# Kernel tuning notes

Measured on AMD Instinct MI355X. Metric: run time of the kernel, lower is better.

## Reference

```python
import jax, jax.numpy as jnp
import numpy as np

B, S = 256, 512
NQ = 1000           # n_skills
MEM, DK, DV, FC = 20, 50, 200, 50  # memory_size, key dim, value dim, final fc dim


def _kaiming(key, shape, fan_in):
    return jax.random.normal(key, shape) * np.float32(np.sqrt(2.0 / fan_in))


def setup_inputs() -> dict:
    key = jax.random.key(0)
    ks = jax.random.split(key, 12)
    q_data = jax.random.randint(ks[0], (B, S), 0, NQ + 1)
    qa_data = jax.random.randint(ks[1], (B, S), 0, 2 * NQ + 1)
    u = jax.random.uniform(ks[2], (B * S,))
    # target: -1 = masked/padding, else binary label (matches target.ge(0) masking)
    target = jnp.where(u < 0.1, -1.0, (u > 0.55).astype(jnp.float32))
    q_embed_w = _kaiming(ks[3], (NQ + 1, DK), DK)
    qa_embed_w = _kaiming(ks[4], (2 * NQ + 1, DV), DV)
    memory_key = _kaiming(ks[5], (MEM, DK), DK)
    init_memory_value = _kaiming(ks[6], (MEM, DV), DV)
    erase_w = _kaiming(ks[7], (DV, DV), DV)
    erase_b = jnp.zeros((DV,), jnp.float32)
    add_w = _kaiming(ks[8], (DV, DV), DV)
    add_b = jnp.zeros((DV,), jnp.float32)
    read_w = _kaiming(ks[9], (DV + FC, FC), DV + FC)
    read_b = jnp.zeros((FC,), jnp.float32)
    pred_w = _kaiming(ks[10], (FC, 1), FC)
    pred_b = jnp.zeros((1,), jnp.float32)
    return dict(q_data=q_data, qa_data=qa_data, target=target,
                q_embed_w=q_embed_w, qa_embed_w=qa_embed_w,
                memory_key=memory_key, init_memory_value=init_memory_value,
                erase_w=erase_w, erase_b=erase_b, add_w=add_w, add_b=add_b,
                read_w=read_w, read_b=read_b, pred_w=pred_w, pred_b=pred_b)


def reference(q_data, qa_data, target, q_embed_w, qa_embed_w, memory_key,
              init_memory_value, erase_w, erase_b, add_w, add_b,
              read_w, read_b, pred_w, pred_b):
    b = q_data.shape[0]
    q_e = q_embed_w[q_data]     # [B,S,DK]
    qa_e = qa_embed_w[qa_data]  # [B,S,DV]
    Mv0 = jnp.broadcast_to(init_memory_value, (b, MEM, DV))

    def step(Mv, xs):
        q_t, qa_t = xs                                        # [B,DK], [B,DV]
        corr = jax.nn.softmax(q_t @ memory_key.T, axis=1)     # [B,MEM] addressing
        read = jnp.einsum('bm,bmd->bd', corr, Mv)             # weighted read
        erase = jax.nn.sigmoid(qa_t @ erase_w + erase_b)      # [B,DV]
        add = jnp.tanh(qa_t @ add_w + add_b)                  # [B,DV]
        w = corr[:, :, None]                                  # [B,MEM,1]
        Mv = Mv * (1.0 - w * erase[:, None, :]) + w * add[:, None, :]
        return Mv, read

    _, reads = jax.lax.scan(step, Mv0, (q_e.transpose(1, 0, 2), qa_e.transpose(1, 0, 2)))
    reads = reads.transpose(1, 0, 2)                          # [B,S,DV]
    x = jnp.concatenate([reads, q_e], axis=-1)                # [B,S,DV+FC]
    h = jnp.tanh(x @ read_w + read_b)                         # [B,S,FC]
    logits = (h @ pred_w + pred_b).reshape(-1)                # [B*S]
    mask = target >= 0.0
    t = jnp.where(mask, target, 0.0)
    # numerically-stable BCE-with-logits, masked mean
    bce = jnp.maximum(logits, 0.0) - logits * t + jnp.log1p(jnp.exp(-jnp.abs(logits)))
    loss = jnp.sum(jnp.where(mask, bce, 0.0)) / jnp.maximum(mask.sum(), 1)
    return loss, jax.nn.sigmoid(logits)
```

## Files before the change

### kernel.cpp

```cpp
#include <hip/hip_runtime.h>
#include <math.h>

#define B_   256
#define S_   512
#define NQ_  1000
#define MEM_ 20
#define DK_  50
#define DV_  200
#define FC_  50
#define RPB  4
#define CHK  16
#define CLEN (S_/CHK)
#define NKS  7
#define XS_STRIDE 232
#define CORR_STRIDE 12
#define NB_EA    ((2*NQ_+1+RPB-1)/RPB)
#define NB_CORR  4
#define NB_WPACK 7
#define NB_HQ    251
#define PREP1_BLOCKS (NB_EA+NB_CORR)
#define MM_BLOCKS (B_*CHK)
#define SCANA_BLOCKS (B_*(CHK-1))
#define SCANA_TOTAL (SCANA_BLOCKS+NB_WPACK+NB_HQ)

typedef __attribute__((ext_vector_type(8))) short bf16x8_t;
typedef __attribute__((ext_vector_type(4))) float f32x4_t;
typedef __attribute__((ext_vector_type(2))) _Float16 f16x2_t;

static __device__ __forceinline__ f16x2_t h2(unsigned u){ return __builtin_bit_cast(f16x2_t, u); }
static __device__ __forceinline__ unsigned h2u(f16x2_t v){ return __builtin_bit_cast(unsigned, v); }
static __device__ __forceinline__ unsigned packh2(float x, float y){
  unsigned short bx = __builtin_bit_cast(unsigned short, (_Float16)x);
  unsigned short by = __builtin_bit_cast(unsigned short, (_Float16)y);
  return (unsigned)bx | ((unsigned)by << 16);
}
static __device__ __forceinline__ f16x2_t pkfma16(f16x2_t a, f16x2_t b, f16x2_t c){
  return __builtin_elementwise_fma(a, b, c);
}

static __device__ __forceinline__ unsigned short f2bf(float f){
  unsigned u = __float_as_uint(f);
  unsigned r = u + 0x7fffu + ((u >> 16) & 1u);
  return (unsigned short)(r >> 16);
}
static __device__ __forceinline__ float ftanh(float x){
  float e = __expf(2.f*x);
  return 1.f - 2.f*__builtin_amdgcn_rcpf(e+1.f);
}
static __device__ __forceinline__ float fsigm(float x){
  return __builtin_amdgcn_rcpf(1.f+__expf(-x));
}

__global__ __launch_bounds__(256) void k_prep1(
    const float* __restrict__ qaw,
    const float* __restrict__ ew, const float* __restrict__ eb,
    const float* __restrict__ aw, const float* __restrict__ ab,
    uint2* __restrict__ eaTab,
    const float* __restrict__ qw, const float* __restrict__ mk,
    unsigned* __restrict__ corrH){
  __shared__ float qa[RPB*DV_];
  int blk = blockIdx.x;
  if(blk < NB_EA){
    int row0 = blk*RPB;
    for(int i=threadIdx.x; i<RPB*DV_; i+=256){
      int r = i/DV_, cc = i - r*DV_;
      int row = row0 + r;
      qa[i] = (row <= 2*NQ_) ? qaw[row*DV_+cc] : 0.f;
    }
    __syncthreads();
    int d = threadIdx.x;
    if(d >= DV_) return;
    float accE[RPB], accA[RPB];
    #pragma unroll
    for(int r=0;r<RPB;++r){ accE[r] = eb[d]; accA[r] = ab[d]; }
    float we0 = ew[d], wa0 = aw[d];
    for(int j=0;j<DV_;++j){
      int jn = (j+1 < DV_) ? j+1 : j;
      float we1 = ew[jn*DV_+d];
      float wa1 = aw[jn*DV_+d];
      #pragma unroll
      for(int r=0;r<RPB;++r){
        float x = qa[r*DV_+j];
        accE[r] = fmaf(x, we0, accE[r]);
        accA[r] = fmaf(x, wa0, accA[r]);
      }
      we0 = we1; wa0 = wa1;
    }
    #pragma unroll
    for(int r=0;r<RPB;++r){
      int row = row0 + r;
      if(row <= 2*NQ_){
        unsigned he = (unsigned)__builtin_bit_cast(unsigned short, (_Float16)fsigm(accE[r]));
        unsigned ha = (unsigned)__builtin_bit_cast(unsigned short, (_Float16)ftanh(accA[r]));
        eaTab[(size_t)row*DV_+d] = make_uint2(he*0x10001u, ha*0x10001u);
      }
    }
  } else {
    int q = (blk-NB_EA)*256 + threadIdx.x;
    if(q > NQ_) return;
    float qv[DK_];
    #pragma unroll
    for(int j=0;j<DK_;++j) qv[j] = qw[q*DK_+j];
    float s[MEM_]; float mx = -1e30f;
    #pragma unroll
    for(int m=0;m<MEM_;++m){
      float acc = 0.f;
      #pragma unroll
      for(int j=0;j<DK_;++j) acc = fmaf(qv[j], mk[m*DK_+j], acc);
      s[m] = acc; mx = fmaxf(mx, acc);
    }
    float sum = 0.f;
    #pragma unroll
    for(int m=0;m<MEM_;++m){ s[m] = __expf(s[m]-mx); sum += s[m]; }
    float inv = __builtin_amdgcn_rcpf(sum);
    #pragma unroll
    for(int i=0;i<MEM_/2;++i)
      corrH[q*CORR_STRIDE+i] = packh2(s[2*i]*inv, s[2*i+1]*inv);
  }
}

__global__ __launch_bounds__(256,8) void k_scanA(const int* __restrict__ qd,
    const int* __restrict__ qad,
    const unsigned* __restrict__ corrH,
    const uint2* __restrict__ eaTab,
    unsigned* __restrict__ ABu,
    const float* __restrict__ qw,
    const float* __restrict__ rw, const float* __restrict__ rb,
    const float* __restrict__ pw,
    unsigned short* __restrict__ WpFrag, float* __restrict__ pwPad,
    float* __restrict__ hq){
  const int blk = blockIdx.x;
  if(blk >= SCANA_BLOCKS){
    int xblk = blk - SCANA_BLOCKS;
    if(xblk < NB_WPACK){
      int ks = xblk;
      int nt = threadIdx.x >> 6;
      int lane = threadIdx.x & 63;
      int quad = lane >> 4, col = lane & 15;
      int n = nt*16 + col;
      unsigned short tmp[8];
      #pragma unroll
      for(int j=0;j<8;++j){
        int k = ks*32 + quad*8 + j;
        tmp[j] = (k < DV_ && n < FC_) ? f2bf(rw[k*FC_+n]) : (unsigned short)0;
      }
      uint4* dst = reinterpret_cast<uint4*>(WpFrag + ((size_t)(ks*4+nt)*64 + lane)*8);
      *dst = *reinterpret_cast<const uint4*>(tmp);
      if(ks == 0 && threadIdx.x < 64)
        pwPad[threadIdx.x] = (threadIdx.x < FC_) ? pw[threadIdx.x] : 0.f;
    } else {
      int idx = (xblk-NB_WPACK)*256 + threadIdx.x;
      int q = idx >> 6, n = idx & 63;
      if(q > NQ_) return;
      float v = 0.f;
      if(n < FC_){
        float acc = rb[n];
        #pragma unroll
        for(int j=0;j<DK_;++j)
          acc = fmaf(qw[q*DK_+j], rw[(DV_+j)*FC_+n], acc);
        v = acc;
      }
      hq[q*64+n] = v;
    }
    return;
  }

  const int b = blk / (CHK-1), c = blk % (CHK-1);
  const int d = threadIdx.x;
  const int dc = (d < DV_) ? d : DV_-1;
  const bool act = (d < DV_);
  const int* __restrict__ qp  = qd  + b*S_ + c*CLEN;
  const int* __restrict__ qap = qad + b*S_ + c*CLEN;

  const f16x2_t one2h = {(_Float16)1.f, (_Float16)1.f};
  f16x2_t A2[MEM_/2], B2[MEM_/2];
  #pragma unroll
  for(int i=0;i<MEM_/2;++i){ A2[i] = one2h; B2[i] = (f16x2_t){(_Float16)0.f,(_Float16)0.f}; }

  int q2   = qp[1];
  int qaT2 = qap[2];
  int qaT3 = qap[3];
  int q1s  = __builtin_amdgcn_readfirstlane(qp[0]);
  const unsigned* cp0 = corrH + q1s*CORR_STRIDE;
  uint4 ca = *(const uint4*)(cp0);
  uint4 cb = *(const uint4*)(cp0+4);
  uint2 cc = *(const uint2*)(cp0+8);
  uint2 ea  = eaTab[(size_t)qap[0]*DV_ + dc];
  uint2 ean = eaTab[(size_t)qap[1]*DV_ + dc];

  #pragma unroll 4
  for(int t=0;t<CLEN;++t){
    int t2 = (t+2 < CLEN) ? t+2 : CLEN-1;
    int t4 = (t+4 < CLEN) ? t+4 : CLEN-1;
    int q3 = qp[t2];
    int qaN = qap[t4];
    int qs = __builtin_amdgcn_readfirstlane(q2);
    const unsigned* cpn_ = corrH + qs*CORR_STRIDE;
    uint4 na = *(const uint4*)(cpn_);
    uint4 nb = *(const uint4*)(cpn_+4);
    uint2 nc = *(const uint2*)(cpn_+8);
    uint2 eann = eaTab[(size_t)qaT2*DV_ + dc];

    const f16x2_t ee = h2(ea.x), aa = h2(ea.y);
    #define UPDA(u, i) { \
      f16x2_t cp = h2(u); \
      f16x2_t al = pkfma16(-cp, ee, one2h); \
      f16x2_t be = cp*aa; \
      A2[i] = A2[i]*al; \
      B2[i] = pkfma16(al, B2[i], be); }
    UPDA(ca.x, 0)  UPDA(ca.y, 1)  UPDA(ca.z, 2)  UPDA(ca.w, 3)
    UPDA(cb.x, 4)  UPDA(cb.y, 5)  UPDA(cb.z, 6)  UPDA(cb.w, 7)
    UPDA(cc.x, 8)  UPDA(cc.y, 9)
    #undef UPDA

    ca=na; cb=nb; cc=nc;
    ea=ean; ean=eann;
    q2=q3; qaT2=qaT3; qaT3=qaN;
  }
  if(act){
    unsigned* base = ABu + ((size_t)(b*(CHK-1) + c)*MEM_)*DV_ + d;
    #pragma unroll
    for(int i=0;i<MEM_/2;++i){
      unsigned a01 = h2u(A2[i]);
      unsigned b01 = h2u(B2[i]);
      base[(size_t)(2*i)*DV_]   = (a01 & 0xffffu) | (b01 << 16);
      base[(size_t)(2*i+1)*DV_] = (a01 >> 16)     | (b01 & 0xffff0000u);
    }
  }
}

__global__ __launch_bounds__(256) void k_prefix(const float* __restrict__ mv0,
    const unsigned* __restrict__ ABu, unsigned* __restrict__ Mv0p){
  int i = blockIdx.x*256 + threadIdx.x;
  if(i >= B_*(MEM_/2)*DV_) return;
  int d = i % DV_;
  int p = (i / DV_) % (MEM_/2);
  int b = i / (DV_*(MEM_/2));
  float MvE = mv0[(2*p)*DV_+d];
  float MvO = mv0[(2*p+1)*DV_+d];
  #pragma unroll
  for(int c=1;c<CHK;++c){
    unsigned vE = ABu[((size_t)(b*(CHK-1) + (c-1))*MEM_ + 2*p)*DV_ + d];
    unsigned vO = ABu[((size_t)(b*(CHK-1) + (c-1))*MEM_ + 2*p+1)*DV_ + d];
    MvE = fmaf((float)h2(vE)[0], MvE, (float)h2(vE)[1]);
    MvO = fmaf((float)h2(vO)[0], MvO, (float)h2(vO)[1]);
    Mv0p[((size_t)(b*CHK + c)*(MEM_/2) + p)*DV_ + d] = packh2(MvE, MvO);
  }
}

__global__ __launch_bounds__(256,8) void k_scan_mm(const int* __restrict__ qd,
    const int* __restrict__ qad,
    const unsigned* __restrict__ corrH,
    const uint2* __restrict__ eaTab,
    const float* __restrict__ mv0,
    const unsigned* __restrict__ Mv0p,
    const unsigned short* __restrict__ WpFrag,
    const float* __restrict__ hq,
    const float* __restrict__ pwPad, const float* __restrict__ pb,
    const float* __restrict__ target,
    float* __restrict__ out, float2* __restrict__ partials){
  __shared__ unsigned short Xs[CLEN*XS_STRIDE];
  __shared__ float sred[2][2][16];
  __shared__ float sbce[4];

  const int blk = blockIdx.x;
  const int b = blk >> 4, c = blk & (CHK-1);
  const int d = threadIdx.x;
  const int dc = (d < DV_) ? d : DV_-1;
  const bool act = (d < DV_);
  const bool padw = (d < 224);
  const int* __restrict__ qp  = qd  + b*S_ + c*CLEN;
  const int* __restrict__ qap = qad + b*S_ + c*CLEN;

  const int wave = threadIdx.x >> 6;
  const int lane = threadIdx.x & 63;
  const int col  = lane & 15, quad = lane >> 4;
  const int rt   = wave & 1;
  const int nh   = wave >> 1;
  const int mbase = rt*16;

  int qpre[4];
  #pragma unroll
  for(int reg=0;reg<4;++reg) qpre[reg] = qp[mbase + quad*4 + reg];

  f16x2_t Mv2[MEM_/2];
  if(c == 0){
    #pragma unroll
    for(int i=0;i<MEM_/2;++i)
      Mv2[i] = (f16x2_t){ (_Float16)mv0[(2*i)*DV_+dc], (_Float16)mv0[(2*i+1)*DV_+dc] };
  } else {
    const unsigned* base = Mv0p + ((size_t)(b*CHK + c)*(MEM_/2))*DV_ + dc;
    #pragma unroll
    for(int i=0;i<MEM_/2;++i)
      Mv2[i] = h2(base[(size_t)i*DV_]);
  }

  int q2   = qp[1];
  int qaT2 = qap[2];
  int qaT3 = qap[3];
  int q1s  = __builtin_amdgcn_readfirstlane(qp[0]);
  const unsigned* cp0 = corrH + q1s*CORR_STRIDE;
  uint4 ca = *(const uint4*)(cp0);
  uint4 cb = *(const uint4*)(cp0+4);
  uint2 cc = *(const uint2*)(cp0+8);
  uint2 ea  = eaTab[(size_t)qap[0]*DV_ + dc];
  uint2 ean = eaTab[(size_t)qap[1]*DV_ + dc];

  #pragma unroll 4
  for(int t=0;t<CLEN;++t){
    int t2 = (t+2 < CLEN) ? t+2 : CLEN-1;
    int t4 = (t+4 < CLEN) ? t+4 : CLEN-1;
    int q3 = qp[t2];
    int qaN = qap[t4];
    int qs = __builtin_amdgcn_readfirstlane(q2);
    const unsigned* cpn_ = corrH + qs*CORR_STRIDE;
    uint4 na = *(const uint4*)(cpn_);
    uint4 nb = *(const uint4*)(cpn_+4);
    uint2 nc = *(const uint2*)(cpn_+8);
    uint2 eann = eaTab[(size_t)qaT2*DV_ + dc];

    const f16x2_t ee = h2(ea.x), aa = h2(ea.y);
    float rd0 = 0.f, rd1 = 0.f;
    #define UPD2(u, i, acc) { \
      f16x2_t cp = h2(u); \
      acc = __builtin_amdgcn_fdot2(cp, Mv2[i], acc, false); \
      f16x2_t tt = pkfma16(-Mv2[i], ee, aa); \
      Mv2[i] = pkfma16(cp, tt, Mv2[i]); }
    UPD2(ca.x, 0, rd0)  UPD2(ca.y, 1, rd1)  UPD2(ca.z, 2, rd0)  UPD2(ca.w, 3, rd1)
    UPD2(cb.x, 4, rd0)  UPD2(cb.y, 5, rd1)  UPD2(cb.z, 6, rd0)  UPD2(cb.w, 7, rd1)
    UPD2(cc.x, 8, rd0)  UPD2(cc.y, 9, rd1)
    #undef UPD2

    if(padw) Xs[t*XS_STRIDE + d] = act ? f2bf(rd0+rd1) : (unsigned short)0;

    ca=na; cb=nb; cc=nc;
    ea=ean; ean=eann;
    q2=q3; qaT2=qaT3; qaT3=qaN;
  }
  __syncthreads();

  float hqv[4][2];
  #pragma unroll
  for(int reg=0;reg<4;++reg)
    #pragma unroll
    for(int j=0;j<2;++j)
      hqv[reg][j] = hq[qpre[reg]*64 + (nh*2+j)*16 + col];

  f32x4_t acc[2];
  acc[0] = (f32x4_t){0.f,0.f,0.f,0.f};
  acc[1] = (f32x4_t){0.f,0.f,0.f,0.f};

  #pragma unroll
  for(int ks=0;ks<NKS;++ks){
    bf16x8_t a = *reinterpret_cast<const bf16x8_t*>(Xs + (mbase+col)*XS_STRIDE + quad*8 + ks*32);
    #pragma unroll
    for(int j=0;j<2;++j){
      int nt = nh*2 + j;
      bf16x8_t bfr = *reinterpret_cast<const bf16x8_t*>(WpFrag + ((size_t)(ks*4+nt)*64 + lane)*8);
      acc[j] = __builtin_amdgcn_mfma_f32_16x16x32_bf16(a, bfr, acc[j], 0, 0, 0);
    }
  }

  float part[4];
  #pragma unroll
  for(int reg=0;reg<4;++reg){
    float s = 0.f;
    #pragma unroll
    for(int j=0;j<2;++j){
      int n = (nh*2+j)*16 + col;
      float h = acc[j][reg] + hqv[reg][j];
      s = fmaf(pwPad[n], ftanh(h), s);
    }
    part[reg] = s;
  }
  #pragma unroll
  for(int off=1; off<16; off<<=1){
    #pragma unroll
    for(int reg=0;reg<4;++reg) part[reg] += __shfl_xor(part[reg], off, 64);
  }
  if(col == 0){
    #pragma unroll
    for(int reg=0;reg<4;++reg) sred[rt][nh][quad*4+reg] = part[reg];
  }
  __syncthreads();

  float bce = 0.f, cnt = 0.f;
  if(nh == 0 && col == 0){
    float pbv = pb[0];
    #pragma unroll
    for(int reg=0;reg<4;++reg){
      int idx = quad*4 + reg;
      int mloc = mbase + idx;
      int row = b*S_ + c*CLEN + mloc;
      float logit = sred[rt][0][idx] + sred[rt][1][idx] + pbv;
      out[1+row] = fsigm(logit);
      float t = target[row];
      if(t >= 0.f){
        cnt += 1.f;
        bce += fmaxf(logit,0.f) - logit*t + log1pf(__expf(-fabsf(logit)));
      }
    }
  }
  bce += __shfl_xor(bce, 16, 64); cnt += __shfl_xor(cnt, 16, 64);
  bce += __shfl_xor(bce, 32, 64); cnt += __shfl_xor(cnt, 32, 64);
  if(lane == 0 && nh == 0){ sbce[wave] = bce; sbce[2+wave] = cnt; }
  __syncthreads();
  if(threadIdx.x == 0)
    partials[blk] = make_float2(sbce[0]+sbce[1], sbce[2]+sbce[3]);
}

__global__ __launch_bounds__(256) void k_fin(const float2* __restrict__ partials,
                                             float* __restrict__ out){
  float bce = 0.f, cnt = 0.f;
  for(int i=threadIdx.x; i<MM_BLOCKS; i+=256){
    float2 p = partials[i];
    bce += p.x; cnt += p.y;
  }
  #pragma unroll
  for(int off=32; off>0; off>>=1){
    bce += __shfl_down(bce, off, 64);
    cnt += __shfl_down(cnt, off, 64);
  }
  __shared__ float sb[4], sc[4];
  int w = threadIdx.x >> 6;
  if((threadIdx.x & 63) == 0){ sb[w] = bce; sc[w] = cnt; }
  __syncthreads();
  if(threadIdx.x == 0){
    float Bt = sb[0]+sb[1]+sb[2]+sb[3];
    float Ct = sc[0]+sc[1]+sc[2]+sc[3];
    out[0] = Bt / fmaxf(Ct, 1.f);
  }
}

extern "C" void kernel_launch(void* const* d_in, const int* in_sizes, int n_in,
                              void* d_out, int out_size, void* d_ws, size_t ws_size,
                              hipStream_t stream){
  const int*   qd     = (const int*)d_in[0];
  const int*   qad    = (const int*)d_in[1];
  const float* target = (const float*)d_in[2];
  const float* qw     = (const float*)d_in[3];
  const float* qaw    = (const float*)d_in[4];
  const float* mk     = (const float*)d_in[5];
  const float* mv0    = (const float*)d_in[6];
  const float* ew     = (const float*)d_in[7];
  const float* eb     = (const float*)d_in[8];
  const float* aw     = (const float*)d_in[9];
  const float* ab     = (const float*)d_in[10];
  const float* rw     = (const float*)d_in[11];
  const float* rb     = (const float*)d_in[12];
  const float* pw     = (const float*)d_in[13];
  const float* pb     = (const float*)d_in[14];
  float* out = (float*)d_out;

  char* ws = (char*)d_ws;
  size_t off = 0;
  float2* partials = (float2*)(ws + off);            off += (size_t)MM_BLOCKS*8;
  unsigned* corrH = (unsigned*)(ws + off);           off += (((size_t)(NQ_+1)*CORR_STRIDE*4 + 255)/256)*256;
  uint2* eaTab    = (uint2*)(ws + off);              off += (((size_t)(2*NQ_+1)*DV_*8 + 255)/256)*256;
  unsigned* ABu   = (unsigned*)(ws + off);           off += (size_t)SCANA_BLOCKS*MEM_*DV_*4;
  unsigned* Mv0p  = (unsigned*)(ws + off);           off += (size_t)MM_BLOCKS*(MEM_/2)*DV_*4;
  unsigned short* WpFrag = (unsigned short*)(ws + off); off += ((size_t)NKS*4*64*8*2 + 255)/256*256;
  float* pwPad    = (float*)(ws + off);              off += 256;
  float* hq       = (float*)(ws + off);              off += (size_t)(NQ_+1)*64*4;

  k_prep1<<<dim3(PREP1_BLOCKS), dim3(256), 0, stream>>>(qaw, ew, eb, aw, ab, eaTab,
                                                        qw, mk, corrH);
  k_scanA<<<dim3(SCANA_TOTAL), dim3(256), 0, stream>>>(qd, qad, corrH, eaTab,
                                                       ABu, qw, rw, rb, pw, WpFrag, pwPad, hq);
  k_prefix<<<dim3((B_*(MEM_/2)*DV_+255)/256), dim3(256), 0, stream>>>(mv0, ABu, Mv0p);
  k_scan_mm<<<dim3(MM_BLOCKS), dim3(256), 0, stream>>>(qd, qad, corrH, eaTab,
                                                       mv0, Mv0p, WpFrag, hq, pwPad, pb, target, out, partials);
  k_fin<<<dim3(1), dim3(256), 0, stream>>>(partials, out);
}
```

Before: 224.1 us.

## Compute erase/add table with bf16 MFMA instead of scalar FMA

Replaces the scalar fp32 per-thread matmul that built the erase/add gate table (2001x200 by 200x400) with a bf16 MFMA kernel. Weights are first packed into MFMA B-fragments (erase and add concatenated along N) in the prep kernel, then a new kernel tiles 32 qa rows per block and applies sigmoid/tanh on the accumulators. This cuts the ALU cost of the table precompute but adds an extra kernel launch and lowers the input precision of the gate computation to bf16.

```diff
diff --git a/kernel.cpp b/kernel.cpp
--- a/kernel.cpp
+++ b/kernel.cpp
@@ -8,17 +8,18 @@
 #define DK_  50
 #define DV_  200
 #define FC_  50
-#define RPB  4
 #define CHK  16
 #define CLEN (S_/CHK)
 #define NKS  7
 #define XS_STRIDE 232
 #define CORR_STRIDE 12
-#define NB_EA    ((2*NQ_+1+RPB-1)/RPB)
+#define EA_NT 28
 #define NB_CORR  4
+#define NB_WPK2  ((NKS*EA_NT+3)/4)
+#define PREP1_BLOCKS (NB_CORR+NB_WPK2)
+#define EA_BLOCKS ((2*NQ_+1+31)/32)
 #define NB_WPACK 7
 #define NB_HQ    251
-#define PREP1_BLOCKS (NB_EA+NB_CORR)
 #define MM_BLOCKS (B_*CHK)
 #define SCANA_BLOCKS (B_*(CHK-1))
 #define SCANA_TOTAL (SCANA_BLOCKS+NB_WPACK+NB_HQ)
@@ -52,51 +53,13 @@
 }
 
 __global__ __launch_bounds__(256) void k_prep1(
-    const float* __restrict__ qaw,
-    const float* __restrict__ ew, const float* __restrict__ eb,
-    const float* __restrict__ aw, const float* __restrict__ ab,
-    uint2* __restrict__ eaTab,
     const float* __restrict__ qw, const float* __restrict__ mk,
-    unsigned* __restrict__ corrH){
-  __shared__ float qa[RPB*DV_];
+    unsigned* __restrict__ corrH,
+    const float* __restrict__ ew, const float* __restrict__ aw,
+    unsigned short* __restrict__ Wfrag2){
   int blk = blockIdx.x;
-  if(blk < NB_EA){
-    int row0 = blk*RPB;
-    for(int i=threadIdx.x; i<RPB*DV_; i+=256){
-      int r = i/DV_, cc = i - r*DV_;
-      int row = row0 + r;
-      qa[i] = (row <= 2*NQ_) ? qaw[row*DV_+cc] : 0.f;
-    }
-    __syncthreads();
-    int d = threadIdx.x;
-    if(d >= DV_) return;
-    float accE[RPB], accA[RPB];
-    #pragma unroll
-    for(int r=0;r<RPB;++r){ accE[r] = eb[d]; accA[r] = ab[d]; }
-    float we0 = ew[d], wa0 = aw[d];
-    for(int j=0;j<DV_;++j){
-      int jn = (j+1 < DV_) ? j+1 : j;
-      float we1 = ew[jn*DV_+d];
-      float wa1 = aw[jn*DV_+d];
-      #pragma unroll
-      for(int r=0;r<RPB;++r){
-        float x = qa[r*DV_+j];
-        accE[r] = fmaf(x, we0, accE[r]);
-        accA[r] = fmaf(x, wa0, accA[r]);
-      }
-      we0 = we1; wa0 = wa1;
-    }
-    #pragma unroll
-    for(int r=0;r<RPB;++r){
-      int row = row0 + r;
-      if(row <= 2*NQ_){
-        unsigned he = (unsigned)__builtin_bit_cast(unsigned short, (_Float16)fsigm(accE[r]));
-        unsigned ha = (unsigned)__builtin_bit_cast(unsigned short, (_Float16)ftanh(accA[r]));
-        eaTab[(size_t)row*DV_+d] = make_uint2(he*0x10001u, ha*0x10001u);
-      }
-    }
-  } else {
-    int q = (blk-NB_EA)*256 + threadIdx.x;
+  if(blk < NB_CORR){
+    int q = blk*256 + threadIdx.x;
     if(q > NQ_) return;
     float qv[DK_];
     #pragma unroll
@@ -116,6 +79,84 @@
     #pragma unroll
     for(int i=0;i<MEM_/2;++i)
       corrH[q*CORR_STRIDE+i] = packh2(s[2*i]*inv, s[2*i+1]*inv);
+  } else {
+    int task = (blk-NB_CORR)*4 + (threadIdx.x >> 6);
+    if(task >= NKS*EA_NT) return;
+    int ks = task / EA_NT, nt = task % EA_NT;
+    int lane = threadIdx.x & 63;
+    int quad = lane >> 4, col = lane & 15;
+    int n = nt*16 + col;
+    unsigned short tmp[8];
+    #pragma unroll
+    for(int j=0;j<8;++j){
+      int k = ks*32 + quad*8 + j;
+      float w = 0.f;
+      if(k < DV_){
+        if(n < DV_)                      w = ew[k*DV_+n];
+        else if(n >= 208 && n < 208+DV_) w = aw[k*DV_+(n-208)];
+      }
+      tmp[j] = f2bf(w);
+    }
+    uint4* dst = reinterpret_cast<uint4*>(Wfrag2 + ((size_t)(ks*EA_NT+nt)*64 + lane)*8);
+    *dst = *reinterpret_cast<const uint4*>(tmp);
+  }
+}
+
+__global__ __launch_bounds__(256) void k_ea_mm(
+    const float* __restrict__ qaw,
+    const float* __restrict__ eb, const float* __restrict__ ab,
+    const unsigned short* __restrict__ Wfrag2,
+    unsigned* __restrict__ eaU){
+  __shared__ unsigned short Xs[32*XS_STRIDE];
+  const int R0 = blockIdx.x*32;
+  for(int i=threadIdx.x; i<32*224; i+=256){
+    int r = i/224, k = i - r*224;
+    int row = R0 + r;
+    float v = (k < DV_ && row <= 2*NQ_) ? qaw[(size_t)row*DV_+k] : 0.f;
+    Xs[r*XS_STRIDE + k] = f2bf(v);
+  }
+  __syncthreads();
+
+  const int wave = threadIdx.x >> 6;
+  const int lane = threadIdx.x & 63;
+  const int col  = lane & 15, quad = lane >> 4;
+  const int rt   = wave & 1;
+  const int nh   = wave >> 1;
+  const int mrow = rt*16;
+
+  for(int nt=nh; nt<EA_NT; nt+=2){
+    f32x4_t acc = (f32x4_t){0.f,0.f,0.f,0.f};
+    #pragma unroll
+    for(int ks=0;ks<NKS;++ks){
+      bf16x8_t a = *reinterpret_cast<const bf16x8_t*>(Xs + (mrow+col)*XS_STRIDE + quad*8 + ks*32);
+      bf16x8_t bfr = *reinterpret_cast<const bf16x8_t*>(Wfrag2 + ((size_t)(ks*EA_NT+nt)*64 + lane)*8);
+      acc = __builtin_amdgcn_mfma_f32_16x16x32_bf16(a, bfr, acc, 0, 0, 0);
+    }
+    int n = nt*16 + col;
+    if(n < DV_){
+      float bias = eb[n];
+      #pragma unroll
+      for(int reg=0;reg<4;++reg){
+        int row = R0 + mrow + quad*4 + reg;
+        if(row <= 2*NQ_){
+          float v = fsigm(acc[reg] + bias);
+          unsigned hv = (unsigned)__builtin_bit_cast(unsigned short, (_Float16)v) * 0x10001u;
+          eaU[((size_t)row*DV_ + n)*2] = hv;
+        }
+      }
+    } else if(n >= 208 && n < 208+DV_){
+      int dd = n - 208;
+      float bias = ab[dd];
+      #pragma unroll
+      for(int reg=0;reg<4;++reg){
+        int row = R0 + mrow + quad*4 + reg;
+        if(row <= 2*NQ_){
+          float v = ftanh(acc[reg] + bias);
+          unsigned hv = (unsigned)__builtin_bit_cast(unsigned short, (_Float16)v) * 0x10001u;
+          eaU[((size_t)row*DV_ + dd)*2 + 1] = hv;
+        }
+      }
+    }
   }
 }
 
@@ -460,11 +501,12 @@
   unsigned* ABu   = (unsigned*)(ws + off);           off += (size_t)SCANA_BLOCKS*MEM_*DV_*4;
   unsigned* Mv0p  = (unsigned*)(ws + off);           off += (size_t)MM_BLOCKS*(MEM_/2)*DV_*4;
   unsigned short* WpFrag = (unsigned short*)(ws + off); off += ((size_t)NKS*4*64*8*2 + 255)/256*256;
+  unsigned short* Wfrag2 = (unsigned short*)(ws + off); off += ((size_t)NKS*EA_NT*64*8*2 + 255)/256*256;
   float* pwPad    = (float*)(ws + off);              off += 256;
   float* hq       = (float*)(ws + off);              off += (size_t)(NQ_+1)*64*4;
 
-  k_prep1<<<dim3(PREP1_BLOCKS), dim3(256), 0, stream>>>(qaw, ew, eb, aw, ab, eaTab,
-                                                        qw, mk, corrH);
+  k_prep1<<<dim3(PREP1_BLOCKS), dim3(256), 0, stream>>>(qw, mk, corrH, ew, aw, Wfrag2);
+  k_ea_mm<<<dim3(EA_BLOCKS), dim3(256), 0, stream>>>(qaw, eb, ab, Wfrag2, (unsigned*)eaTab);
   k_scanA<<<dim3(SCANA_TOTAL), dim3(256), 0, stream>>>(qd, qad, corrH, eaTab,
                                                        ABu, qw, rw, rb, pw, WpFrag, pwPad, hq);
   k_prefix<<<dim3((B_*(MEM_/2)*DV_+255)/256), dim3(256), 0, stream>>>(mv0, ABu, Mv0p);
```

Measured after the change: 258.2 us. +15.2%, slower.
